# Kernel optimization log

Hardware: AMD Instinct MI355X
Metric: run time of the kernel (lower is better)

## Reference

```python
import jax, jax.numpy as jnp
import numpy as np

T, N, CIN, C, B, G, GG = 3, 200000, 256, 256, 512, 64, 256
H = 2 * GG  # graph_global_channels * 2
EPS = 1e-5


def setup_inputs() -> dict:
    key = jax.random.key(0)
    ks = jax.random.split(key, 32)
    r = lambda i, s: jax.random.normal(ks[i], s, dtype=jnp.float32)
    return {
        "x": r(1, (T, N, CIN)),
        "global_attr": r(2, (B, G)),
        "Wl": r(3, (T, CIN, C)), "bl": r(4, (T, C)),
        "Wr": r(5, (T, C, C)), "br": r(6, (T, C)),
        "att": r(7, (T, C)), "bias_out": r(8, (T, C)),
        "gtok": jnp.zeros((T, C), jnp.float32),  # global tokens init to zeros as in source
        "mix1_pw": r(9, (G + 3 * C, H)), "mix1_pb": r(10, (H,)),
        "mix1_w1": r(11, (G + 3 * C, H)), "mix1_b1": r(12, (H,)),
        "mix1_w2": r(13, (H, H)), "mix1_b2": r(14, (H,)),
        "bn1_g": jnp.ones((H,), jnp.float32), "bn1_b": jnp.zeros((H,), jnp.float32),
        "mix2_w1": r(15, (H, H)), "mix2_b1": r(16, (H,)),
        "mix2_w2": r(17, (H, H)), "mix2_b2": r(18, (H,)),
        "bn2_g": jnp.ones((H,), jnp.float32), "bn2_b": jnp.zeros((H,), jnp.float32),
        "mix3_pw": r(19, (H, GG)), "mix3_pb": r(20, (GG,)),
        "mix3_w1": r(21, (H, GG)), "mix3_b1": r(22, (GG,)),
        "mix3_w2": r(23, (GG, GG)), "mix3_b2": r(24, (GG,)),
        "batch": jnp.sort(jax.random.randint(ks[0], (T, N), 0, B), axis=1),
    }


def _bn(x, g, b):
    # BatchNorm1d in training mode (biased variance over batch dim)
    mu = jnp.mean(x, 0)
    var = jnp.mean((x - mu) ** 2, 0)
    return (x - mu) * jax.lax.rsqrt(var + EPS) * g + b


def _gatv2(x, batch, Wl, bl, Wr, br, att, gtok, bias_out):
    # GATv2Conv, heads=1, bipartite (nodes -> per-graph global token), add_self_loops=False
    xl = jnp.einsum('tnc,tcd->tnd', x, Wl) + bl[:, None, :]  # source transform [T,N,C]
    xr = jnp.einsum('tc,tcd->td', gtok, Wr) + br             # dest token transform, same for every graph [T,C]
    s = jax.nn.leaky_relu(xl + xr[:, None, :], negative_slope=0.2)
    e = jnp.sum(s * att[:, None, :], axis=-1)                # [T,N] edge logits (one edge per node)

    def seg(e_t, xl_t, b_t):
        m = jax.ops.segment_max(e_t, b_t, num_segments=B)
        ex = jnp.exp(e_t - m[b_t])
        den = jax.ops.segment_sum(ex, b_t, num_segments=B)
        alpha = ex / jnp.where(den[b_t] > 0, den[b_t], 1.0)  # per-graph softmax
        return jax.ops.segment_sum(alpha[:, None] * xl_t, b_t, num_segments=B)

    out = jax.vmap(seg)(e, xl, batch)  # [T,B,C]
    return out + bias_out[:, None, :]


def reference(x, global_attr, Wl, bl, Wr, br, att, bias_out, gtok,
              mix1_pw, mix1_pb, mix1_w1, mix1_b1, mix1_w2, mix1_b2, bn1_g, bn1_b,
              mix2_w1, mix2_b1, mix2_w2, mix2_b2, bn2_g, bn2_b,
              mix3_pw, mix3_pb, mix3_w1, mix3_b1, mix3_w2, mix3_b2, batch):
    g = _gatv2(x, batch, Wl, bl, Wr, br, att, gtok, bias_out)  # [T,B,C]
    h = jnp.concatenate([global_attr, g[0], g[1], g[2]], axis=1)  # [B, G+3C]
    # ResidualLinear(832 -> 512) + BN + Tanh
    h = (h @ mix1_pw + mix1_pb) + (jnp.tanh(h @ mix1_w1 + mix1_b1) @ mix1_w2 + mix1_b2)
    h = jnp.tanh(_bn(h, bn1_g, bn1_b))
    # ResidualLinear(512 -> 512, identity projection) + BN + Tanh
    h = h + (jnp.tanh(h @ mix2_w1 + mix2_b1) @ mix2_w2 + mix2_b2)
    h = jnp.tanh(_bn(h, bn2_g, bn2_b))
    # ResidualLinear(512 -> 256)
    h = (h @ mix3_pw + mix3_pb) + (jnp.tanh(h @ mix3_w1 + mix3_b1) @ mix3_w2 + mix3_b2)
    return (g, h)
```

## Files before the change

kernel.cpp:

```cpp
#include <hip/hip_runtime.h>
#include <hip/hip_bf16.h>

typedef __bf16 bf16x8 __attribute__((ext_vector_type(8)));
typedef float  f32x4  __attribute__((ext_vector_type(4)));

#define T_   3
#define N_   200000
#define C_   256
#define B_   512
#define EPSb 1e-5f

__device__ __forceinline__ unsigned enc_f(float f){
  unsigned u = __float_as_uint(f);
  return (u & 0x80000000u) ? ~u : (u | 0x80000000u);
}
__device__ __forceinline__ float dec_f(unsigned k){
  unsigned u = (k & 0x80000000u) ? (k ^ 0x80000000u) : ~k;
  return __uint_as_float(u);
}
__device__ __forceinline__ float ftanh(float x){
  float e = __expf(2.0f*x);
  return 1.0f - 2.0f/(e + 1.0f);
}

__device__ __forceinline__ void barrier_nodrain(){
  __builtin_amdgcn_sched_barrier(0);
  asm volatile("s_waitcnt lgkmcnt(0)" ::: "memory");
  __builtin_amdgcn_s_barrier();
  __builtin_amdgcn_sched_barrier(0);
}

__global__ void kprep(const float* __restrict__ Wl, __hip_bfloat16* __restrict__ wlt,
                      const float* __restrict__ Wr, const float* __restrict__ bl,
                      const float* __restrict__ br, const float* __restrict__ gtok,
                      float* __restrict__ cvec, float* __restrict__ zr){
  __shared__ float tile[64][65];
  __shared__ float gt[256];
  int blk = blockIdx.x, tid = threadIdx.x;
  if (blk < 48){
    int t = blk / 16, rem = blk % 16;
    int k0 = (rem >> 2)*64, c0 = (rem & 3)*64;
    int lc = tid & 63, lr0 = tid >> 6;
    #pragma unroll
    for (int q = 0; q < 16; q++){
      int lr = lr0*16 + q;
      tile[lr][lc] = Wl[t*65536 + (k0+lr)*256 + (c0+lc)];
    }
    __syncthreads();
    #pragma unroll
    for (int q = 0; q < 16; q++){
      int lr = lr0*16 + q;
      wlt[t*65536 + (c0+lr)*256 + (k0+lc)] = __float2bfloat16(tile[lc][lr]);
    }
  } else if (blk < 51){
    int t = blk - 48, c = tid;
    gt[tid] = gtok[t*256 + tid];
    __syncthreads();
    const float* wr = Wr + t*65536 + c;
    float a0=0.f,a1=0.f,a2=0.f,a3=0.f;
    #pragma unroll 2
    for (int k = 0; k < 256; k += 4){
      a0 += gt[k]  *wr[k*256];
      a1 += gt[k+1]*wr[(k+1)*256];
      a2 += gt[k+2]*wr[(k+2)*256];
      a3 += gt[k+3]*wr[(k+3)*256];
    }
    cvec[t*256 + c] = a0+a1+a2+a3 + bl[t*256+c] + br[t*256+c];
  } else {
    for (int i = (blk-51)*256 + tid; i < 398336; i += (gridDim.x-51)*256) zr[i] = 0.f;
  }
}

__global__ __launch_bounds__(512, 2)
void k1(const float* __restrict__ x, const __hip_bfloat16* __restrict__ wlt,
        const float* __restrict__ cvec, const float* __restrict__ att,
        const int* __restrict__ batch, float* __restrict__ e_out,
        unsigned* __restrict__ mkey){
  __shared__ __align__(16) __hip_bfloat16 Abuf[64][256];
  __shared__ float elds[4][64];
  const int tid = threadIdx.x;
  const int w = tid >> 6, l = tid & 63;
  const int wcol = w & 3, wrow = w >> 2;
  const int l15 = l & 15, l4 = l >> 4;
  const int srow = tid >> 3;
  const int sc   = tid & 7;
  const int sx   = srow & 7;

  bf16x8 bfr[8][4];
  float cv[4], at[4];
  int cur_t = -1;

  const int bid = blockIdx.x;
  const int nt = 18 + (bid < 159 ? 1 : 0);
  const int g0 = bid*18 + (bid < 159 ? bid : 159);

  f32x4 rg[8];
  {
    int t = g0 / 3125, tile = g0 % 3125;
    const float* xrow = x + (size_t)t*N_*256 + (size_t)(tile*64 + srow)*256;
    #pragma unroll
    for (int q = 0; q < 4; q++){
      int cs = (q*8 + sc) ^ sx;
      rg[2*q]   = *(const f32x4*)(xrow + cs*8);
      rg[2*q+1] = *(const f32x4*)(xrow + cs*8 + 4);
    }
  }

  for (int it = 0; it < nt; ++it){
    const int gt = g0 + it;
    const int t = gt / 3125, tile = gt % 3125;
    if (t != cur_t){
      cur_t = t;
      const __hip_bfloat16* WT = wlt + t*65536;
      #pragma unroll
      for (int fn = 0; fn < 4; fn++){
        int col = wcol*64 + fn*16 + l15;
        cv[fn] = cvec[t*256 + col];
        at[fn] = att[t*256 + col];
        #pragma unroll
        for (int ks = 0; ks < 8; ks++)
          bfr[ks][fn] = *(const bf16x8*)(WT + col*256 + ks*32 + l4*8);
      }
    }
    #pragma unroll
    for (int q = 0; q < 4; q++){
      bf16x8 v;
      #pragma unroll
      for (int j = 0; j < 4; j++){ v[j] = (__bf16)rg[2*q][j]; v[4+j] = (__bf16)rg[2*q+1][j]; }
      *(bf16x8*)(&Abuf[srow][(q*8 + sc)*8]) = v;
    }
    if (it + 1 < nt){
      int gn = gt + 1;
      int tn = gn / 3125, tilen = gn % 3125;
      const float* xrow = x + (size_t)tn*N_*256 + (size_t)(tilen*64 + srow)*256;
      #pragma unroll
      for (int q = 0; q < 4; q++){
        int cs = (q*8 + sc) ^ sx;
        rg[2*q]   = *(const f32x4*)(xrow + cs*8);
        rg[2*q+1] = *(const f32x4*)(xrow + cs*8 + 4);
      }
    }
    barrier_nodrain();

    f32x4 acc[2][4];
    #pragma unroll
    for (int fm = 0; fm < 2; fm++)
      #pragma unroll
      for (int fn = 0; fn < 4; fn++)
        acc[fm][fn] = (f32x4){0.f,0.f,0.f,0.f};

    #pragma unroll
    for (int ks = 0; ks < 8; ks++){
      bf16x8 a8[2];
      #pragma unroll
      for (int fm = 0; fm < 2; fm++){
        int row  = wrow*32 + fm*16 + l15;
        int slot = (ks*4 + l4) ^ (row & 7);
        a8[fm] = *(const bf16x8*)(&Abuf[row][slot*8]);
      }
      #pragma unroll
      for (int fm = 0; fm < 2; fm++)
        #pragma unroll
        for (int fn = 0; fn < 4; fn++)
          acc[fm][fn] = __builtin_amdgcn_mfma_f32_16x16x32_bf16(a8[fm], bfr[ks][fn], acc[fm][fn], 0, 0, 0);
    }

    #pragma unroll
    for (int fm = 0; fm < 2; fm++){
      #pragma unroll
      for (int r = 0; r < 4; r++){
        float v = 0.f;
        #pragma unroll
        for (int fn = 0; fn < 4; fn++){
          float xv = acc[fm][fn][r] + cv[fn];
          xv = (xv > 0.f) ? xv : 0.2f*xv;
          v += xv * at[fn];
        }
        v += __shfl_xor(v, 1);
        v += __shfl_xor(v, 2);
        v += __shfl_xor(v, 4);
        v += __shfl_xor(v, 8);
        if (l15 == 0) elds[wcol][wrow*32 + fm*16 + l4*4 + r] = v;
      }
    }
    barrier_nodrain();

    if (tid < 64){
      float ef = elds[0][tid] + elds[1][tid] + elds[2][tid] + elds[3][tid];
      int n = tile*64 + tid;
      e_out[t*N_ + n] = ef;
      int b = batch[t*N_ + n];
      float m = ef;
      #pragma unroll
      for (int off = 1; off < 64; off <<= 1){
        float up = __shfl_up(m, off);
        int   bu = __shfl_up(b, off);
        if (tid >= off && bu == b) m = fmaxf(m, up);
      }
      int bnx = __shfl_down(b, 1);
      if (tid == 63 || b != bnx) atomicMax(&mkey[t*B_ + b], enc_f(m));
    }
  }
}

__global__ void kscan(const float* __restrict__ x, const float* __restrict__ Wl,
                      const float* __restrict__ cvec, const float* __restrict__ att,
                      const int* __restrict__ batch, const float* __restrict__ e,
                      const unsigned* __restrict__ mkey,
                      float* __restrict__ den, float* __restrict__ gacc){
  __shared__ float xs[256];
  __shared__ float red[4];
  __shared__ float ebc;
  __shared__ int hits[256];
  __shared__ int nh;
  int t = blockIdx.y;
  int tid = threadIdx.x;
  int n0 = blockIdx.x*256;
  int n = n0 + tid;
  if (tid == 0) nh = 0;
  __syncthreads();
  if (n < N_){
    float ev = e[t*N_ + n];
    int b = batch[t*N_ + n];
    float m = dec_f(mkey[t*B_ + b]);
    if (ev >= m - 30.0f){ int p = atomicAdd(&nh, 1); hits[p] = tid; }
  }
  __syncthreads();
  int cnum = nh;
  for (int i = 0; i < cnum; i++){
    int hn = n0 + hits[i];
    xs[tid] = x[(size_t)t*N_*256 + (size_t)hn*256 + tid];
    __syncthreads();
    const float* wp = Wl + t*65536 + tid;
    float a0 = 0.f, a1 = 0.f;
    #pragma unroll 8
    for (int k = 0; k < 256; k += 2){
      a0 += xs[k]   * wp[k*256];
      a1 += xs[k+1] * wp[(k+1)*256];
    }
    float xl = a0 + a1;
    float xv = xl + cvec[t*256 + tid];
    xv = (xv > 0.f) ? xv : 0.2f*xv;
    float term = xv * att[t*256 + tid];
    #pragma unroll
    for (int off = 1; off < 64; off <<= 1) term += __shfl_xor(term, off);
    if ((tid & 63) == 0) red[tid >> 6] = term;
    __syncthreads();
    if (tid == 0) ebc = red[0] + red[1] + red[2] + red[3];
    __syncthreads();
    int b = batch[t*N_ + hn];
    float m = dec_f(mkey[t*B_ + b]);
    float wv = expf(ebc - m);
    if (tid == 0) atomicAdd(&den[t*B_ + b], wv);
    atomicAdd(&gacc[t*131072 + b*256 + tid], wv * xl);
    __syncthreads();
  }
}

__global__ void kgfinal(const float* __restrict__ gacc, const float* __restrict__ den,
                        const float* __restrict__ bl, const float* __restrict__ bout,
                        float* __restrict__ gout){
  int i = blockIdx.x*256 + threadIdx.x;
  if (i >= 393216) return;
  int t = i >> 17, b = (i >> 8) & 511, c = i & 255;
  float d = den[t*B_ + b];
  float v = (d > 0.f) ? gacc[i]/d + bl[t*256+c] : 0.f;
  gout[i] = v + bout[t*256 + c];
}

__device__ __forceinline__ void load_stage(const float* __restrict__ A,
    const float* __restrict__ W, const float* __restrict__ ga,
    const float* __restrict__ gfin, int aMode, int K, int N,
    int row0, int col0, int arow, int akq, int wcol, int wkg, int s,
    float* av, float* wv){
  int kg = (s << 6) + akq*16;
  const float* p;
  if (aMode == 0)      p = A + (size_t)(row0+arow)*K + kg;
  else if (aMode == 1) p = (kg < 64) ? ga + (size_t)(row0+arow)*64 + kg
                         : gfin + (size_t)((kg-64) >> 8)*131072 + (size_t)(row0+arow)*256 + ((kg-64) & 255);
  else                 p = A + (size_t)(row0+arow)*512 + kg;
  #pragma unroll
  for (int q = 0; q < 4; q++){
    f32x4 v = *(const f32x4*)(p + q*4);
    av[q*4+0]=v[0]; av[q*4+1]=v[1]; av[q*4+2]=v[2]; av[q*4+3]=v[3];
  }
  const float* q = W + (size_t)((s << 6) + wkg*16)*N + col0 + wcol;
  #pragma unroll
  for (int j = 0; j < 16; j++) wv[j] = q[(size_t)j*N];
}

__global__ __launch_bounds__(256)
void kmfma(const float* __restrict__ A, const float* __restrict__ addsrc,
           const float* __restrict__ ga, const float* __restrict__ gfin,
           const float* __restrict__ bnsums, const float* __restrict__ bng,
           const float* __restrict__ bnb, float* __restrict__ stats,
           const float* __restrict__ W0, const float* __restrict__ bias0,
           float* __restrict__ out0, int tanh0,
           const float* __restrict__ W1, const float* __restrict__ bias1,
           float* __restrict__ out1, int tanh1,
           int N, int K, int aMode, int addMode){
  __shared__ __align__(16) __bf16 As[2][64][72];
  __shared__ __align__(16) __bf16 Ws[2][64][72];
  __shared__ float bnsc[512], bnsh[512];
  __shared__ float reds[16][64];

  const float* W = W0; const float* bias = bias0; float* out = out0; int dotanh = tanh0;
  if (blockIdx.z){ W = W1; bias = bias1; out = out1; dotanh = tanh1; }

  const int tid = threadIdx.x;
  const int w = tid >> 6, l = tid & 63;
  const int l15 = l & 15, l4 = l >> 4;
  const int row0 = blockIdx.y*64, col0 = blockIdx.x*64;
  const int arow = tid >> 2, akq = tid & 3;
  const int wcol = tid & 63, wkg = tid >> 6;

  if (aMode == 2 || addMode == 2){
    #pragma unroll
    for (int q = 0; q < 2; q++){
      int k = q*256 + tid;
      float mu = bnsums[k] * (1.f/512.f);
      float var = bnsums[512+k] * (1.f/512.f) - mu*mu;
      float sc = bng[k] * __frsqrt_rn(var + EPSb);
      bnsc[k] = sc;
      bnsh[k] = bnb[k] - mu*sc;
    }
    __syncthreads();
  }

  f32x4 acc[4];
  #pragma unroll
  for (int cf = 0; cf < 4; cf++) acc[cf] = (f32x4){0.f,0.f,0.f,0.f};

  const int nk = K >> 6;
  float avr[16], wvr[16];
  load_stage(A, W, ga, gfin, aMode, K, N, row0, col0, arow, akq, wcol, wkg, 0, avr, wvr);

  for (int s = 0; s < nk; s++){
    int kgA = (s << 6) + akq*16;
    bf16x8 ah[2], al[2], wh[2], wl[2];
    #pragma unroll
    for (int half = 0; half < 2; half++){
      #pragma unroll
      for (int j = 0; j < 8; j++){
        float vv = avr[half*8 + j];
        if (aMode == 2) vv = ftanh(vv*bnsc[kgA + half*8 + j] + bnsh[kgA + half*8 + j]);
        __bf16 h = (__bf16)vv;
        ah[half][j] = h;
        al[half][j] = (__bf16)(vv - (float)h);
        float wvv = wvr[half*8 + j];
        __bf16 wh_ = (__bf16)wvv;
        wh[half][j] = wh_;
        wl[half][j] = (__bf16)(wvv - (float)wh_);
      }
    }
    *(bf16x8*)&As[0][arow][akq*16]     = ah[0];
    *(bf16x8*)&As[0][arow][akq*16 + 8] = ah[1];
    *(bf16x8*)&As[1][arow][akq*16]     = al[0];
    *(bf16x8*)&As[1][arow][akq*16 + 8] = al[1];
    *(bf16x8*)&Ws[0][wcol][wkg*16]     = wh[0];
    *(bf16x8*)&Ws[0][wcol][wkg*16 + 8] = wh[1];
    *(bf16x8*)&Ws[1][wcol][wkg*16]     = wl[0];
    *(bf16x8*)&Ws[1][wcol][wkg*16 + 8] = wl[1];
    if (s + 1 < nk)
      load_stage(A, W, ga, gfin, aMode, K, N, row0, col0, arow, akq, wcol, wkg, s+1, avr, wvr);
    barrier_nodrain();

    #pragma unroll
    for (int h = 0; h < 2; h++){
      bf16x8 afh = *(const bf16x8*)&As[0][w*16 + l15][h*32 + l4*8];
      bf16x8 afl = *(const bf16x8*)&As[1][w*16 + l15][h*32 + l4*8];
      #pragma unroll
      for (int cf = 0; cf < 4; cf++){
        bf16x8 bfh = *(const bf16x8*)&Ws[0][cf*16 + l15][h*32 + l4*8];
        bf16x8 bfl = *(const bf16x8*)&Ws[1][cf*16 + l15][h*32 + l4*8];
        acc[cf] = __builtin_amdgcn_mfma_f32_16x16x32_bf16(afh, bfh, acc[cf], 0, 0, 0);
        acc[cf] = __builtin_amdgcn_mfma_f32_16x16x32_bf16(afh, bfl, acc[cf], 0, 0, 0);
        acc[cf] = __builtin_amdgcn_mfma_f32_16x16x32_bf16(afl, bfh, acc[cf], 0, 0, 0);
      }
    }
    barrier_nodrain();
  }

  float vsum[4], vsq[4];
  #pragma unroll
  for (int cf = 0; cf < 4; cf++){ vsum[cf] = 0.f; vsq[cf] = 0.f; }
  #pragma unroll
  for (int cf = 0; cf < 4; cf++){
    int col = col0 + cf*16 + l15;
    #pragma unroll
    for (int r = 0; r < 4; r++){
      int row = row0 + w*16 + l4*4 + r;
      float v = acc[cf][r] + bias[col];
      if (addMode == 1) v += addsrc[(size_t)row*N + col];
      else if (addMode == 2) v += ftanh(addsrc[(size_t)row*512 + col]*bnsc[col] + bnsh[col]);
      if (dotanh) v = ftanh(v);
      out[(size_t)row*N + col] = v;
      vsum[cf] += v;
      vsq[cf]  += v*v;
    }
  }

  if (stats){
    __syncthreads();
    #pragma unroll
    for (int cf = 0; cf < 4; cf++) reds[w*4 + l4][cf*16 + l15] = vsum[cf];
    __syncthreads();
    if (tid < 64){
      float s = 0.f;
      #pragma unroll
      for (int r = 0; r < 16; r++) s += reds[r][tid];
      atomicAdd(&stats[col0 + tid], s);
    }
    __syncthreads();
    #pragma unroll
    for (int cf = 0; cf < 4; cf++) reds[w*4 + l4][cf*16 + l15] = vsq[cf];
    __syncthreads();
    if (tid < 64){
      float s = 0.f;
      #pragma unroll
      for (int r = 0; r < 16; r++) s += reds[r][tid];
      atomicAdd(&stats[512 + col0 + tid], s);
    }
  }
}

extern "C" void kernel_launch(void* const* d_in, const int* in_sizes, int n_in,
                              void* d_out, int out_size, void* d_ws, size_t ws_size,
                              hipStream_t stream){
  const float* x    = (const float*)d_in[0];
  const float* ga   = (const float*)d_in[1];
  const float* Wl   = (const float*)d_in[2];
  const float* bl   = (const float*)d_in[3];
  const float* Wr   = (const float*)d_in[4];
  const float* br   = (const float*)d_in[5];
  const float* att  = (const float*)d_in[6];
  const float* bout = (const float*)d_in[7];
  const float* gtok = (const float*)d_in[8];
  const float* m1pw = (const float*)d_in[9];
  const float* m1pb = (const float*)d_in[10];
  const float* m1w1 = (const float*)d_in[11];
  const float* m1b1 = (const float*)d_in[12];
  const float* m1w2 = (const float*)d_in[13];
  const float* m1b2 = (const float*)d_in[14];
  const float* bn1g = (const float*)d_in[15];
  const float* bn1b = (const float*)d_in[16];
  const float* m2w1 = (const float*)d_in[17];
  const float* m2b1 = (const float*)d_in[18];
  const float* m2w2 = (const float*)d_in[19];
  const float* m2b2 = (const float*)d_in[20];
  const float* bn2g = (const float*)d_in[21];
  const float* bn2b = (const float*)d_in[22];
  const float* m3pw = (const float*)d_in[23];
  const float* m3pb = (const float*)d_in[24];
  const float* m3w1 = (const float*)d_in[25];
  const float* m3b1 = (const float*)d_in[26];
  const float* m3w2 = (const float*)d_in[27];
  const float* m3b2 = (const float*)d_in[28];
  const int*   batch= (const int*)d_in[29];

  float* gout = (float*)d_out;
  float* hout = (float*)d_out + 393216;

  char* w = (char*)d_ws;
  __hip_bfloat16* wlt = (__hip_bfloat16*)(w + 0);
  float*    cvec = (float*)(w + 393216);
  float*    ebuf = (float*)(w + 396288);
  float*    gacc = (float*)(w + 2796288);
  float*    den  = (float*)(w + 4369152);
  unsigned* mkey = (unsigned*)(w + 4375296);
  float*    bns  = (float*)(w + 4381440);
  float*    T1   = (float*)(w + 4389632);
  float*    P1   = (float*)(w + 5438208);
  float*    Hm   = (float*)(w + 6486784);
  float*    T2   = (float*)(w + 7535360);
  float*    H2   = (float*)(w + 8583936);
  float*    T3   = (float*)(w + 9632512);
  float*    P3   = (float*)(w + 10156800);

  kprep<<<435, 256, 0, stream>>>(Wl, wlt, Wr, bl, br, gtok, cvec, gacc);
  k1<<<512, 512, 0, stream>>>(x, wlt, cvec, att, batch, ebuf, mkey);
  kscan<<<dim3(782, 3), 256, 0, stream>>>(x, Wl, cvec, att, batch, ebuf, mkey, den, gacc);
  kgfinal<<<1536, 256, 0, stream>>>(gacc, den, bl, bout, gout);
  kmfma<<<dim3(8,8,2), 256, 0, stream>>>(nullptr, nullptr, ga, gout,
      nullptr, nullptr, nullptr, nullptr,
      m1w1, m1b1, T1, 1, m1pw, m1pb, P1, 0, 512, 832, 1, 0);
  kmfma<<<dim3(8,8,1), 256, 0, stream>>>(T1, P1, nullptr, nullptr,
      nullptr, nullptr, nullptr, bns,
      m1w2, m1b2, Hm, 0, nullptr, nullptr, nullptr, 0, 512, 512, 0, 1);
  kmfma<<<dim3(8,8,1), 256, 0, stream>>>(Hm, nullptr, nullptr, nullptr,
      bns, bn1g, bn1b, nullptr,
      m2w1, m2b1, T2, 1, nullptr, nullptr, nullptr, 0, 512, 512, 2, 0);
  kmfma<<<dim3(8,8,1), 256, 0, stream>>>(T2, Hm, nullptr, nullptr,
      bns, bn1g, bn1b, bns + 1024,
      m2w2, m2b2, H2, 0, nullptr, nullptr, nullptr, 0, 512, 512, 0, 2);
  kmfma<<<dim3(4,8,2), 256, 0, stream>>>(H2, nullptr, nullptr, nullptr,
      bns + 1024, bn2g, bn2b, nullptr,
      m3w1, m3b1, T3, 1, m3pw, m3pb, P3, 0, 256, 512, 2, 0);
  kmfma<<<dim3(4,8,1), 256, 0, stream>>>(T3, P3, nullptr, nullptr,
      nullptr, nullptr, nullptr, nullptr,
      m3w2, m3b2, hout, 0, nullptr, nullptr, nullptr, 0, 256, 256, 0, 1);
}
```

Measured before the change: 379.6 us.

## Stream x tiles into double-buffered LDS via async global-to-LDS loads

In k1, x tiles are now loaded straight from global memory into a double-buffered fp32 LDS buffer using global_load_lds. This replaces the register staging and the early bf16 conversion, and the conversion to bf16 now happens when fragments are read from LDS. The grid is halved to 256 blocks, each handling twice as many tiles, and the two-blocks-per-CU launch bound is dropped. The goal is to overlap the next tile's fetch with the current MFMA work and to free the registers used for staging. The cost is 128KB of LDS per block, which limits occupancy to one block per CU, plus extra conversion work on every LDS read.

```diff
diff --git a/kernel.cpp b/kernel.cpp
--- a/kernel.cpp
+++ b/kernel.cpp
@@ -28,6 +28,12 @@
   asm volatile("s_waitcnt lgkmcnt(0)" ::: "memory");
   __builtin_amdgcn_s_barrier();
   __builtin_amdgcn_sched_barrier(0);
+}
+
+__device__ __forceinline__ void gload_lds16(const float* src, float* lds_dst){
+  __builtin_amdgcn_global_load_lds(
+      (const __attribute__((address_space(1))) unsigned*)src,
+      (__attribute__((address_space(3))) unsigned*)lds_dst, 16, 0, 0);
 }
 
 __global__ void kprep(const float* __restrict__ Wl, __hip_bfloat16* __restrict__ wlt,
@@ -71,38 +77,33 @@
   }
 }
 
-__global__ __launch_bounds__(512, 2)
+__global__ __launch_bounds__(512)
 void k1(const float* __restrict__ x, const __hip_bfloat16* __restrict__ wlt,
         const float* __restrict__ cvec, const float* __restrict__ att,
         const int* __restrict__ batch, float* __restrict__ e_out,
         unsigned* __restrict__ mkey){
-  __shared__ __align__(16) __hip_bfloat16 Abuf[64][256];
+  __shared__ __align__(16) float Af[2][64][256];
   __shared__ float elds[4][64];
   const int tid = threadIdx.x;
   const int w = tid >> 6, l = tid & 63;
   const int wcol = w & 3, wrow = w >> 2;
   const int l15 = l & 15, l4 = l >> 4;
-  const int srow = tid >> 3;
-  const int sc   = tid & 7;
-  const int sx   = srow & 7;
 
   bf16x8 bfr[8][4];
   float cv[4], at[4];
   int cur_t = -1;
 
   const int bid = blockIdx.x;
-  const int nt = 18 + (bid < 159 ? 1 : 0);
-  const int g0 = bid*18 + (bid < 159 ? bid : 159);
-
-  f32x4 rg[8];
+  const int nt = 36 + (bid < 159 ? 1 : 0);
+  const int g0 = bid*36 + (bid < 159 ? bid : 159);
+
   {
-    int t = g0 / 3125, tile = g0 % 3125;
-    const float* xrow = x + (size_t)t*N_*256 + (size_t)(tile*64 + srow)*256;
-    #pragma unroll
-    for (int q = 0; q < 4; q++){
-      int cs = (q*8 + sc) ^ sx;
-      rg[2*q]   = *(const f32x4*)(xrow + cs*8);
-      rg[2*q+1] = *(const f32x4*)(xrow + cs*8 + 4);
+    int t0 = g0 / 3125, tile0 = g0 % 3125;
+    const float* xb = x + (size_t)t0*N_*256 + (size_t)tile0*64*256;
+    #pragma unroll
+    for (int i = 0; i < 8; i++){
+      int r = w*8 + i;
+      gload_lds16(xb + (size_t)r*256 + ((l ^ i) << 2), &Af[0][r][0]);
     }
   }
 
@@ -122,25 +123,28 @@
           bfr[ks][fn] = *(const bf16x8*)(WT + col*256 + ks*32 + l4*8);
       }
     }
-    #pragma unroll
-    for (int q = 0; q < 4; q++){
-      bf16x8 v;
-      #pragma unroll
-      for (int j = 0; j < 4; j++){ v[j] = (__bf16)rg[2*q][j]; v[4+j] = (__bf16)rg[2*q+1][j]; }
-      *(bf16x8*)(&Abuf[srow][(q*8 + sc)*8]) = v;
-    }
+    const float* Ab = &Af[it & 1][0][0];
+
     if (it + 1 < nt){
       int gn = gt + 1;
       int tn = gn / 3125, tilen = gn % 3125;
-      const float* xrow = x + (size_t)tn*N_*256 + (size_t)(tilen*64 + srow)*256;
-      #pragma unroll
-      for (int q = 0; q < 4; q++){
-        int cs = (q*8 + sc) ^ sx;
-        rg[2*q]   = *(const f32x4*)(xrow + cs*8);
-        rg[2*q+1] = *(const f32x4*)(xrow + cs*8 + 4);
-      }
-    }
-    barrier_nodrain();
+      const float* xb = x + (size_t)tn*N_*256 + (size_t)tilen*64*256;
+      float* Dn = &Af[(it+1) & 1][0][0];
+      #pragma unroll
+      for (int i = 0; i < 8; i++){
+        int r = w*8 + i;
+        gload_lds16(xb + (size_t)r*256 + ((l ^ i) << 2), Dn + r*256);
+      }
+      __builtin_amdgcn_sched_barrier(0);
+      asm volatile("s_waitcnt vmcnt(8)" ::: "memory");
+      __builtin_amdgcn_sched_barrier(0);
+    } else {
+      __builtin_amdgcn_sched_barrier(0);
+      asm volatile("s_waitcnt vmcnt(0)" ::: "memory");
+      __builtin_amdgcn_sched_barrier(0);
+    }
+    __builtin_amdgcn_s_barrier();
+    __builtin_amdgcn_sched_barrier(0);
 
     f32x4 acc[2][4];
     #pragma unroll
@@ -154,9 +158,14 @@
       bf16x8 a8[2];
       #pragma unroll
       for (int fm = 0; fm < 2; fm++){
-        int row  = wrow*32 + fm*16 + l15;
-        int slot = (ks*4 + l4) ^ (row & 7);
-        a8[fm] = *(const bf16x8*)(&Abuf[row][slot*8]);
+        int row = wrow*32 + fm*16 + l15;
+        int sxr = row & 7;
+        int c0 = ks*8 + l4*2;
+        const float* rp = Ab + row*256;
+        f32x4 p0 = *(const f32x4*)(rp + (((c0    ) ^ sxr) << 2));
+        f32x4 p1 = *(const f32x4*)(rp + (((c0 + 1) ^ sxr) << 2));
+        #pragma unroll
+        for (int j = 0; j < 4; j++){ a8[fm][j] = (__bf16)p0[j]; a8[fm][4+j] = (__bf16)p1[j]; }
       }
       #pragma unroll
       for (int fm = 0; fm < 2; fm++)
@@ -478,7 +487,7 @@
   float*    P3   = (float*)(w + 10156800);
 
   kprep<<<435, 256, 0, stream>>>(Wl, wlt, Wr, bl, br, gtok, cvec, gacc);
-  k1<<<512, 512, 0, stream>>>(x, wlt, cvec, att, batch, ebuf, mkey);
+  k1<<<256, 512, 0, stream>>>(x, wlt, cvec, att, batch, ebuf, mkey);
   kscan<<<dim3(782, 3), 256, 0, stream>>>(x, Wl, cvec, att, batch, ebuf, mkey, den, gacc);
   kgfinal<<<1536, 256, 0, stream>>>(gacc, den, bl, bout, gout);
   kmfma<<<dim3(8,8,2), 256, 0, stream>>>(nullptr, nullptr, ga, gout,
```

Result: no change. 375.6 us (median of 2 runs) (-1.0%).
